# Kernel optimization log

Measured on AMD Instinct MI355X. Metric: run time of the kernel, lower is better.

The kernel has to match this reference:

```python
import jax, jax.numpy as jnp
import numpy as np

B, S, D, H = 8, 1024, 1024, 16
HD = D // H  # head dim = 64


def setup_inputs() -> dict:
    key = jax.random.key(0)
    ks = jax.random.split(key, 8)
    return {
        "hidden_states": jax.random.normal(ks[0], (B, S, D), dtype=jnp.float32),
        "attention_mask": jnp.zeros((B, 1, 1, S), dtype=jnp.float32),
        "Wq": jax.random.normal(ks[1], (D, D), dtype=jnp.float32) * (1.0 / np.sqrt(D)),
        "bq": jax.random.normal(ks[2], (D,), dtype=jnp.float32) * 0.02,
        "Wk": jax.random.normal(ks[3], (D, D), dtype=jnp.float32) * (1.0 / np.sqrt(D)),
        "bk": jax.random.normal(ks[4], (D,), dtype=jnp.float32) * 0.02,
        "Wv": jax.random.normal(ks[5], (D, D), dtype=jnp.float32) * (1.0 / np.sqrt(D)),
        "bv": jax.random.normal(ks[6], (D,), dtype=jnp.float32) * 0.02,
    }


def _split_heads(x):
    # [B,S,D] -> [B,H,S,HD]
    return x.reshape(B, S, H, HD).transpose(0, 2, 1, 3)


def reference(hidden_states, attention_mask, Wq, bq, Wk, bk, Wv, bv):
    q = _split_heads(hidden_states @ Wq + bq)
    k = _split_heads(hidden_states @ Wk + bk)
    v = _split_heads(hidden_states @ Wv + bv)
    # [B,H,S,S]
    scores = jnp.einsum("bhqd,bhkd->bhqk", q, k) / jnp.sqrt(jnp.float32(HD))
    scores = scores + attention_mask
    probs = jax.nn.softmax(scores, axis=-1)  # dropout p=0.0 (eval)
    ctx = jnp.einsum("bhqk,bhkd->bhqd", probs, v)
    # [B,H,S,HD] -> [B,S,D]
    return ctx.transpose(0, 2, 1, 3).reshape(B, S, D)
```

## Files before the change

kernel.cpp:

```cpp
#include <hip/hip_runtime.h>
#include <stdint.h>

#define BB 8
#define SS 1024
#define DD 1024
#define HH 16
#define HDIM 64

typedef __bf16 bf16x8 __attribute__((ext_vector_type(8)));
typedef float f32x4 __attribute__((ext_vector_type(4)));

__device__ __forceinline__ unsigned short f2bf(float f) {
    union { float f; unsigned u; } v; v.f = f;
    unsigned r = v.u + 0x7fff + ((v.u >> 16) & 1);
    return (unsigned short)(r >> 16);
}

__device__ __forceinline__ float exp2fast(float x) {
#if __has_builtin(__builtin_amdgcn_exp2f)
    return __builtin_amdgcn_exp2f(x);
#else
    return __expf(x * 0.69314718f);
#endif
}

__device__ __forceinline__ void async16(void* lds, const void* g) {
    __builtin_amdgcn_global_load_lds(
        (const __attribute__((address_space(1))) unsigned int*)g,
        (__attribute__((address_space(3))) unsigned int*)lds, 16, 0, 0);
}

__global__ __launch_bounds__(256) void prep(
    const float* __restrict__ x, unsigned short* __restrict__ xf,
    const float* __restrict__ w0, const float* __restrict__ w1,
    const float* __restrict__ w2,
    unsigned short* __restrict__ f0, unsigned short* __restrict__ f1,
    unsigned short* __restrict__ f2)
{
    __shared__ unsigned short tile[64 * 76];
    int bid = blockIdx.x;
    int tid = threadIdx.x;
    if (bid < 2048) {
        int mt = bid >> 4, kt = bid & 15;
        const float* src = x + (size_t)(mt * 64) * DD + kt * 64;
        #pragma unroll
        for (int i = 0; i < 4; ++i) {
            int f = tid + i * 256;
            int r = f >> 4, c4 = f & 15;
            float4 v = *reinterpret_cast<const float4*>(src + r * DD + c4 * 4);
            ushort4 o;
            o.x = f2bf(v.x); o.y = f2bf(v.y); o.z = f2bf(v.z); o.w = f2bf(v.w);
            *reinterpret_cast<ushort4*>(&tile[r * 76 + c4 * 4]) = o;
        }
        __syncthreads();
        #pragma unroll
        for (int i = 0; i < 2; ++i) {
            int s = tid + i * 256;
            int frag = s >> 6, l = s & 63;
            int m_l = (frag & 3) * 16 + (l & 15);
            int k_l = (frag >> 2) * 32 + ((l >> 4) & 3) * 8;
            uint4 v = *reinterpret_cast<const uint4*>(&tile[m_l * 76 + k_l]);
            int fm = mt * 4 + (frag & 3);
            int fk = kt * 2 + (frag >> 2);
            *reinterpret_cast<uint4*>(xf + (size_t)((fm * 32 + fk) * 64 + l) * 8) = v;
        }
        return;
    }
    int idx = bid - 2048;
    int z = idx >> 8, rem = idx & 255;
    const float* w = (z == 0) ? w0 : (z == 1) ? w1 : w2;
    unsigned short* wf = (z == 0) ? f0 : (z == 1) ? f1 : f2;
    int kt = rem & 15, nt = rem >> 4;
    const float* src = w + (size_t)(kt * 64) * DD + nt * 64;
    #pragma unroll
    for (int i = 0; i < 4; ++i) {
        int f = tid + i * 256;
        int r = f >> 4, c4 = f & 15;
        float4 v = *reinterpret_cast<const float4*>(src + r * DD + c4 * 4);
        ushort4 o;
        o.x = f2bf(v.x); o.y = f2bf(v.y); o.z = f2bf(v.z); o.w = f2bf(v.w);
        *reinterpret_cast<ushort4*>(&tile[r * 76 + c4 * 4]) = o;
    }
    __syncthreads();
    #pragma unroll
    for (int i = 0; i < 2; ++i) {
        int s = tid + i * 256;
        int frag = s >> 6, l = s & 63;
        int n_l = (frag & 3) * 16 + (l & 15);
        int k_l = (frag >> 2) * 32 + ((l >> 4) & 3) * 8;
        unsigned short tmp[8];
        #pragma unroll
        for (int j = 0; j < 8; ++j) tmp[j] = tile[(k_l + j) * 76 + n_l];
        int fn = nt * 4 + (frag & 3);
        int fk = kt * 2 + (frag >> 2);
        *reinterpret_cast<uint4*>(wf + (size_t)((fn * 32 + fk) * 64 + l) * 8) =
            *reinterpret_cast<const uint4*>(tmp);
    }
}

__global__ __launch_bounds__(256, 3) void gemm_qkv(
    const unsigned short* __restrict__ xf,
    const unsigned short* __restrict__ wf0, const unsigned short* __restrict__ wf1,
    const unsigned short* __restrict__ wf2,
    const float* __restrict__ b0, const float* __restrict__ b1, const float* __restrict__ b2,
    unsigned short* __restrict__ qo, unsigned short* __restrict__ ko,
    unsigned short* __restrict__ vto)
{
    int bid = blockIdx.x;
    int xcd = bid & 7, g = bid >> 3;
    int strip = xcd * 3 + (g % 3);
    int mt = g / 3;
    int nt = strip & 7, z = strip >> 3;

    const unsigned short* wf; const float* bias; unsigned short* out;
    if (z == 0)      { wf = wf0; bias = b0; out = qo; }
    else if (z == 1) { wf = wf1; bias = b1; out = ko; }
    else             { wf = wf2; bias = b2; out = vto; }

    __shared__ unsigned short stg[4][64 * 76];

    int tid = threadIdx.x;
    int wave = tid >> 6, lane = tid & 63, lq = lane >> 4, lm = lane & 15;
    int wr = wave >> 1, wc = wave & 1;

    const unsigned short* aB = xf + (size_t)((mt * 8 + wr * 4) * 32) * 512 + lane * 8;
    const unsigned short* bB = wf + (size_t)((nt * 8 + wc * 4) * 32) * 512 + lane * 8;

    f32x4 acc[4][4] = {};
    bf16x8 a0[4], a1[4], bb0[4], bb1[4];

#define LDFRAGS(AB, BB, T)                                                     \
    {                                                                          \
        _Pragma("unroll") for (int i_ = 0; i_ < 4; ++i_)                       \
            AB[i_] = *reinterpret_cast<const bf16x8*>(aB + (i_ * 32 + (T)) * 512); \
        _Pragma("unroll") for (int j_ = 0; j_ < 4; ++j_)                       \
            BB[j_] = *reinterpret_cast<const bf16x8*>(bB + (j_ * 32 + (T)) * 512); \
    }
#define MFMAS(AB, BB)                                                          \
    {                                                                          \
        _Pragma("unroll") for (int i_ = 0; i_ < 4; ++i_)                       \
            _Pragma("unroll") for (int j_ = 0; j_ < 4; ++j_)                   \
                acc[i_][j_] = __builtin_amdgcn_mfma_f32_16x16x32_bf16(         \
                    AB[i_], BB[j_], acc[i_][j_], 0, 0, 0);                     \
    }

    LDFRAGS(a0, bb0, 0);
    for (int tt = 0; tt < 16; ++tt) {
        int t = tt * 2;
        LDFRAGS(a1, bb1, t + 1);
        MFMAS(a0, bb0);
        LDFRAGS(a0, bb0, t + 2);
        MFMAS(a1, bb1);
    }
#undef LDFRAGS
#undef MFMAS

    int m0 = mt * 128;
    int col0 = nt * 128 + wc * 64;
    if (z == 2) {
        #pragma unroll
        for (int j = 0; j < 4; ++j) {
            int col = col0 + j * 16 + lm;
            float bsv = bias[col];
            int h = col >> 6, hd = col & 63;
            #pragma unroll
            for (int i = 0; i < 4; ++i) {
                int m = m0 + wr * 64 + i * 16 + lq * 4;
                int b_ = m >> 10, sr = m & 1023;
                union { float f; unsigned u; } p0, p1, p2, p3;
                p0.f = acc[i][j][0] + bsv; p1.f = acc[i][j][1] + bsv;
                p2.f = acc[i][j][2] + bsv; p3.f = acc[i][j][3] + bsv;
                uint2 pk;
                pk.x = __builtin_amdgcn_perm(p1.u + 0x8000u, p0.u + 0x8000u, 0x07060302u);
                pk.y = __builtin_amdgcn_perm(p3.u + 0x8000u, p2.u + 0x8000u, 0x07060302u);
                *reinterpret_cast<uint2*>(out + (((b_ * HH + h) * HDIM + hd) << 10) + sr) = pk;
            }
        }
    } else {
        unsigned short* S = stg[wave];
        #pragma unroll
        for (int j = 0; j < 4; ++j) {
            float bsv = bias[col0 + j * 16 + lm];
            #pragma unroll
            for (int i = 0; i < 4; ++i) {
                #pragma unroll
                for (int r = 0; r < 4; ++r) {
                    union { float f; unsigned u; } cv; cv.f = acc[i][j][r] + bsv;
                    S[(i * 16 + lq * 4 + r) * 76 + j * 16 + lm] =
                        (unsigned short)((cv.u + 0x8000u) >> 16);
                }
            }
        }
        int h = col0 >> 6;
        int mrow = m0 + wr * 64;
        int b_ = mrow >> 10, sr0 = mrow & 1023;
        unsigned short* ob = out + ((size_t)((b_ * HH + h) << 10) + sr0) * HDIM;
        #pragma unroll
        for (int u = 0; u < 8; ++u) {
            int s = lane + u * 64;
            int row = s >> 3, c8 = s & 7;
            uint4 v = *reinterpret_cast<const uint4*>(&S[row * 76 + c8 * 8]);
            *reinterpret_cast<uint4*>(ob + row * HDIM + c8 * 8) = v;
        }
    }
}

__global__ __launch_bounds__(256) void attention(
    const unsigned short* __restrict__ q,
    const unsigned short* __restrict__ k,
    const unsigned short* __restrict__ vt,
    const float* __restrict__ mask,
    float* __restrict__ out)
{
    __shared__ unsigned short Ks[2][64 * 64];
    __shared__ unsigned short Vs[2][64 * 64];
    __shared__ unsigned short Ps[4][16 * 72];
    __shared__ float msk[SS];

    int blk = blockIdx.x;
    int xcd = blk & 7, j = blk >> 3;
    int bh = (xcd << 4) + (j >> 4);
    int qt = j & 15;
    int b = bh >> 4, h = bh & 15;

    int tid = threadIdx.x;
    int wave = tid >> 6, lane = tid & 63, lq = lane >> 4, lm = lane & 15;

    const unsigned short* qp = q + (size_t)bh * SS * HDIM;
    const unsigned short* kp = k + (size_t)bh * SS * HDIM;
    const unsigned short* vp = vt + (size_t)bh * HDIM * SS;

    for (int i = tid; i < SS; i += 256) msk[i] = mask[b * SS + i] * 1.44269504f;

    int qrow = qt * 64 + wave * 16 + lm;
    bf16x8 qa0 = *reinterpret_cast<const bf16x8*>(qp + qrow * HDIM + lq * 8);
    bf16x8 qa1 = *reinterpret_cast<const bf16x8*>(qp + qrow * HDIM + 32 + lq * 8);

    float lsum = 0.f;
    f32x4 o[4] = {};

    int row0 = tid >> 3, sg = tid & 7;
    int cg = (sg - row0) & 7;
    const unsigned short* gk = kp + row0 * 64 + cg * 8;
    const unsigned short* gv = vp + row0 * SS + cg * 8;

    int sl0 = ((lq + lm) & 7) * 8;
    int sl1 = ((lq + lm + 4) & 7) * 8;

    async16(&Ks[0][tid * 8], gk);  async16(&Ks[0][(tid + 256) * 8], gk + 32 * 64);
    async16(&Vs[0][tid * 8], gv);  async16(&Vs[0][(tid + 256) * 8], gv + 32 * SS);
    gk += 64 * 64; gv += 64;

    unsigned short* Pw = Ps[wave];

    for (int t = 0; t < 16; ++t) {
        int p = t & 1;
        __syncthreads();
        if (t < 15) {
            async16(&Ks[p ^ 1][tid * 8], gk);  async16(&Ks[p ^ 1][(tid + 256) * 8], gk + 32 * 64);
            async16(&Vs[p ^ 1][tid * 8], gv);  async16(&Vs[p ^ 1][(tid + 256) * 8], gv + 32 * SS);
            gk += 64 * 64; gv += 64;
        }
        int kb0 = t * 64;

        f32x4 c[4];
        #pragma unroll
        for (int nb = 0; nb < 4; ++nb) {
            bf16x8 kf0 = *reinterpret_cast<const bf16x8*>(&Ks[p][(nb * 16 + lm) * 64 + sl0]);
            bf16x8 kf1 = *reinterpret_cast<const bf16x8*>(&Ks[p][(nb * 16 + lm) * 64 + sl1]);
            f32x4 z = {};
            z = __builtin_amdgcn_mfma_f32_16x16x32_bf16(kf0, qa0, z, 0, 0, 0);
            z = __builtin_amdgcn_mfma_f32_16x16x32_bf16(kf1, qa1, z, 0, 0, 0);
            c[nb] = z;
        }

        #pragma unroll
        for (int nb = 0; nb < 4; ++nb) {
            float4 mk = *reinterpret_cast<const float4*>(&msk[kb0 + nb * 16 + lq * 4]);
            unsigned u[4];
            #pragma unroll
            for (int r = 0; r < 4; ++r) {
                float e = exp2fast(fmaf(c[nb][r], 0.18033688f,
                                        reinterpret_cast<const float*>(&mk)[r]));
                union { float f; unsigned v; } cv; cv.f = e;
                u[r] = cv.v;
                union { unsigned v; float f; } tr; tr.v = cv.v & 0xffff0000u;
                lsum += tr.f;
            }
            uint2 pk;
            pk.x = __builtin_amdgcn_perm(u[1], u[0], 0x07060302u);
            pk.y = __builtin_amdgcn_perm(u[3], u[2], 0x07060302u);
            *reinterpret_cast<uint2*>(&Pw[lm * 72 + nb * 16 + lq * 4]) = pk;
        }

        #pragma unroll
        for (int ks = 0; ks < 2; ++ks) {
            bf16x8 pa = *reinterpret_cast<const bf16x8*>(&Pw[lm * 72 + ks * 32 + lq * 8]);
            int slv = (ks == 0) ? sl0 : sl1;
            #pragma unroll
            for (int nb2 = 0; nb2 < 4; ++nb2) {
                bf16x8 vf = *reinterpret_cast<const bf16x8*>(&Vs[p][(nb2 * 16 + lm) * 64 + slv]);
                o[nb2] = __builtin_amdgcn_mfma_f32_16x16x32_bf16(pa, vf, o[nb2], 0, 0, 0);
            }
        }
    }

    lsum += __shfl_xor(lsum, 16, 64);
    lsum += __shfl_xor(lsum, 32, 64);
    float linv[4];
    #pragma unroll
    for (int r = 0; r < 4; ++r)
        linv[r] = 1.0f / __shfl(lsum, lq * 4 + r, 64);

    #pragma unroll
    for (int nb2 = 0; nb2 < 4; ++nb2) {
        #pragma unroll
        for (int r = 0; r < 4; ++r) {
            int sr = qt * 64 + wave * 16 + lq * 4 + r;
            out[((size_t)(b * SS + sr)) * DD + h * HDIM + nb2 * 16 + lm] = o[nb2][r] * linv[r];
        }
    }
}

extern "C" void kernel_launch(void* const* d_in, const int* in_sizes, int n_in,
                              void* d_out, int out_size, void* d_ws, size_t ws_size,
                              hipStream_t stream) {
    const float* hs   = (const float*)d_in[0];
    const float* mask = (const float*)d_in[1];
    const float* Wq   = (const float*)d_in[2];
    const float* bq   = (const float*)d_in[3];
    const float* Wk   = (const float*)d_in[4];
    const float* bk   = (const float*)d_in[5];
    const float* Wv   = (const float*)d_in[6];
    const float* bv   = (const float*)d_in[7];
    float* out = (float*)d_out;

    char* ws = (char*)d_ws;
    unsigned short* XF  = (unsigned short*)(ws);
    unsigned short* WF0 = (unsigned short*)(ws + 16777216);
    unsigned short* WF1 = (unsigned short*)(ws + 18874368);
    unsigned short* WF2 = (unsigned short*)(ws + 20971520);
    unsigned short* qw  = (unsigned short*)(ws + 23068672);
    unsigned short* kw  = (unsigned short*)(ws + 39845888);
    unsigned short* vtw = (unsigned short*)(ws + 56623104);

    prep<<<2816, 256, 0, stream>>>(hs, XF, Wq, Wk, Wv, WF0, WF1, WF2);
    gemm_qkv<<<1536, 256, 0, stream>>>(XF, WF0, WF1, WF2,
                                       bq, bk, bv, qw, kw, vtw);
    attention<<<2048, 256, 0, stream>>>(qw, kw, vtw, mask, out);
}
```

Baseline: 232.6 us.

## Process two query tiles per attention block to halve K/V staging traffic

Each attention block now handles 128 query rows (two 16-row groups per wave) instead of 64, so every K/V tile staged in shared memory feeds twice as many MFMAs, and the grid is halved. The mask is read from global memory each iteration instead of being cached in shared memory. The P scratch buffer is narrowed to a 64-wide row with an XOR-style swizzle in place of 72-wide padding. A launch-bounds occupancy hint is added. The extra accumulators raise register pressure, and the smaller grid gives fewer blocks to fill the GPU.

```diff
diff --git a/kernel.cpp b/kernel.cpp
--- a/kernel.cpp
+++ b/kernel.cpp
@@ -205,7 +205,7 @@
     }
 }
 
-__global__ __launch_bounds__(256) void attention(
+__global__ __launch_bounds__(256, 4) void attention(
     const unsigned short* __restrict__ q,
     const unsigned short* __restrict__ k,
     const unsigned short* __restrict__ vt,
@@ -214,13 +214,12 @@
 {
     __shared__ unsigned short Ks[2][64 * 64];
     __shared__ unsigned short Vs[2][64 * 64];
-    __shared__ unsigned short Ps[4][16 * 72];
-    __shared__ float msk[SS];
+    __shared__ unsigned short Ps[4][16 * 64];
 
     int blk = blockIdx.x;
     int xcd = blk & 7, j = blk >> 3;
-    int bh = (xcd << 4) + (j >> 4);
-    int qt = j & 15;
+    int bh = (xcd << 4) + (j >> 3);
+    int qt = j & 7;
     int b = bh >> 4, h = bh & 15;
 
     int tid = threadIdx.x;
@@ -229,15 +228,16 @@
     const unsigned short* qp = q + (size_t)bh * SS * HDIM;
     const unsigned short* kp = k + (size_t)bh * SS * HDIM;
     const unsigned short* vp = vt + (size_t)bh * HDIM * SS;
-
-    for (int i = tid; i < SS; i += 256) msk[i] = mask[b * SS + i] * 1.44269504f;
-
-    int qrow = qt * 64 + wave * 16 + lm;
-    bf16x8 qa0 = *reinterpret_cast<const bf16x8*>(qp + qrow * HDIM + lq * 8);
-    bf16x8 qa1 = *reinterpret_cast<const bf16x8*>(qp + qrow * HDIM + 32 + lq * 8);
-
-    float lsum = 0.f;
-    f32x4 o[4] = {};
+    const float* maskb = mask + b * SS;
+
+    int qbase = qt * 128 + wave * 16 + lm;
+    bf16x8 qa00 = *reinterpret_cast<const bf16x8*>(qp + qbase * HDIM + lq * 8);
+    bf16x8 qa01 = *reinterpret_cast<const bf16x8*>(qp + qbase * HDIM + 32 + lq * 8);
+    bf16x8 qa10 = *reinterpret_cast<const bf16x8*>(qp + (qbase + 64) * HDIM + lq * 8);
+    bf16x8 qa11 = *reinterpret_cast<const bf16x8*>(qp + (qbase + 64) * HDIM + 32 + lq * 8);
+
+    float lsum0 = 0.f, lsum1 = 0.f;
+    f32x4 o0[4] = {}, o1[4] = {};
 
     int row0 = tid >> 3, sg = tid & 7;
     int cg = (sg - row0) & 7;
@@ -246,78 +246,123 @@
 
     int sl0 = ((lq + lm) & 7) * 8;
     int sl1 = ((lq + lm + 4) & 7) * 8;
+    unsigned short* Pw = Ps[wave];
+    int pwbase = lm * 64 + (lq & 1) * 4;
+    int prd0 = lm * 64 + sl0;
+    int prd1 = lm * 64 + sl1;
 
     async16(&Ks[0][tid * 8], gk);  async16(&Ks[0][(tid + 256) * 8], gk + 32 * 64);
     async16(&Vs[0][tid * 8], gv);  async16(&Vs[0][(tid + 256) * 8], gv + 32 * SS);
     gk += 64 * 64; gv += 64;
 
-    unsigned short* Pw = Ps[wave];
-
     for (int t = 0; t < 16; ++t) {
         int p = t & 1;
         __syncthreads();
+        int kb0 = t * 64;
+
+        float4 mk[4];
+        #pragma unroll
+        for (int nb = 0; nb < 4; ++nb) {
+            mk[nb] = *reinterpret_cast<const float4*>(maskb + kb0 + nb * 16 + lq * 4);
+            #pragma unroll
+            for (int r = 0; r < 4; ++r)
+                reinterpret_cast<float*>(&mk[nb])[r] *= 1.44269504f;
+        }
         if (t < 15) {
             async16(&Ks[p ^ 1][tid * 8], gk);  async16(&Ks[p ^ 1][(tid + 256) * 8], gk + 32 * 64);
             async16(&Vs[p ^ 1][tid * 8], gv);  async16(&Vs[p ^ 1][(tid + 256) * 8], gv + 32 * SS);
             gk += 64 * 64; gv += 64;
         }
-        int kb0 = t * 64;
-
-        f32x4 c[4];
+
+        f32x4 c0[4], c1[4];
         #pragma unroll
         for (int nb = 0; nb < 4; ++nb) {
             bf16x8 kf0 = *reinterpret_cast<const bf16x8*>(&Ks[p][(nb * 16 + lm) * 64 + sl0]);
             bf16x8 kf1 = *reinterpret_cast<const bf16x8*>(&Ks[p][(nb * 16 + lm) * 64 + sl1]);
             f32x4 z = {};
-            z = __builtin_amdgcn_mfma_f32_16x16x32_bf16(kf0, qa0, z, 0, 0, 0);
-            z = __builtin_amdgcn_mfma_f32_16x16x32_bf16(kf1, qa1, z, 0, 0, 0);
-            c[nb] = z;
+            z = __builtin_amdgcn_mfma_f32_16x16x32_bf16(kf0, qa00, z, 0, 0, 0);
+            z = __builtin_amdgcn_mfma_f32_16x16x32_bf16(kf1, qa01, z, 0, 0, 0);
+            c0[nb] = z;
+            f32x4 w = {};
+            w = __builtin_amdgcn_mfma_f32_16x16x32_bf16(kf0, qa10, w, 0, 0, 0);
+            w = __builtin_amdgcn_mfma_f32_16x16x32_bf16(kf1, qa11, w, 0, 0, 0);
+            c1[nb] = w;
         }
 
         #pragma unroll
         for (int nb = 0; nb < 4; ++nb) {
-            float4 mk = *reinterpret_cast<const float4*>(&msk[kb0 + nb * 16 + lq * 4]);
             unsigned u[4];
             #pragma unroll
             for (int r = 0; r < 4; ++r) {
-                float e = exp2fast(fmaf(c[nb][r], 0.18033688f,
-                                        reinterpret_cast<const float*>(&mk)[r]));
+                float e = exp2fast(fmaf(c0[nb][r], 0.18033688f,
+                                        reinterpret_cast<const float*>(&mk[nb])[r]));
                 union { float f; unsigned v; } cv; cv.f = e;
                 u[r] = cv.v;
                 union { unsigned v; float f; } tr; tr.v = cv.v & 0xffff0000u;
-                lsum += tr.f;
+                lsum0 += tr.f;
             }
             uint2 pk;
             pk.x = __builtin_amdgcn_perm(u[1], u[0], 0x07060302u);
             pk.y = __builtin_amdgcn_perm(u[3], u[2], 0x07060302u);
-            *reinterpret_cast<uint2*>(&Pw[lm * 72 + nb * 16 + lq * 4]) = pk;
-        }
-
-        #pragma unroll
-        for (int ks = 0; ks < 2; ++ks) {
-            bf16x8 pa = *reinterpret_cast<const bf16x8*>(&Pw[lm * 72 + ks * 32 + lq * 8]);
-            int slv = (ks == 0) ? sl0 : sl1;
-            #pragma unroll
-            for (int nb2 = 0; nb2 < 4; ++nb2) {
-                bf16x8 vf = *reinterpret_cast<const bf16x8*>(&Vs[p][(nb2 * 16 + lm) * 64 + slv]);
-                o[nb2] = __builtin_amdgcn_mfma_f32_16x16x32_bf16(pa, vf, o[nb2], 0, 0, 0);
+            *reinterpret_cast<uint2*>(
+                &Pw[pwbase + (((nb * 2 + (lq >> 1)) + lm) & 7) * 8]) = pk;
+        }
+        bf16x8 pa00 = *reinterpret_cast<const bf16x8*>(&Pw[prd0]);
+        bf16x8 pa01 = *reinterpret_cast<const bf16x8*>(&Pw[prd1]);
+
+        #pragma unroll
+        for (int nb = 0; nb < 4; ++nb) {
+            unsigned u[4];
+            #pragma unroll
+            for (int r = 0; r < 4; ++r) {
+                float e = exp2fast(fmaf(c1[nb][r], 0.18033688f,
+                                        reinterpret_cast<const float*>(&mk[nb])[r]));
+                union { float f; unsigned v; } cv; cv.f = e;
+                u[r] = cv.v;
+                union { unsigned v; float f; } tr; tr.v = cv.v & 0xffff0000u;
+                lsum1 += tr.f;
             }
-        }
-    }
-
-    lsum += __shfl_xor(lsum, 16, 64);
-    lsum += __shfl_xor(lsum, 32, 64);
-    float linv[4];
+            uint2 pk;
+            pk.x = __builtin_amdgcn_perm(u[1], u[0], 0x07060302u);
+            pk.y = __builtin_amdgcn_perm(u[3], u[2], 0x07060302u);
+            *reinterpret_cast<uint2*>(
+                &Pw[pwbase + (((nb * 2 + (lq >> 1)) + lm) & 7) * 8]) = pk;
+        }
+        bf16x8 pa10 = *reinterpret_cast<const bf16x8*>(&Pw[prd0]);
+        bf16x8 pa11 = *reinterpret_cast<const bf16x8*>(&Pw[prd1]);
+
+        #pragma unroll
+        for (int nb2 = 0; nb2 < 4; ++nb2) {
+            bf16x8 vf0 = *reinterpret_cast<const bf16x8*>(&Vs[p][(nb2 * 16 + lm) * 64 + sl0]);
+            o0[nb2] = __builtin_amdgcn_mfma_f32_16x16x32_bf16(pa00, vf0, o0[nb2], 0, 0, 0);
+            o1[nb2] = __builtin_amdgcn_mfma_f32_16x16x32_bf16(pa10, vf0, o1[nb2], 0, 0, 0);
+            bf16x8 vf1 = *reinterpret_cast<const bf16x8*>(&Vs[p][(nb2 * 16 + lm) * 64 + sl1]);
+            o0[nb2] = __builtin_amdgcn_mfma_f32_16x16x32_bf16(pa01, vf1, o0[nb2], 0, 0, 0);
+            o1[nb2] = __builtin_amdgcn_mfma_f32_16x16x32_bf16(pa11, vf1, o1[nb2], 0, 0, 0);
+        }
+    }
+
+    lsum0 += __shfl_xor(lsum0, 16, 64);
+    lsum0 += __shfl_xor(lsum0, 32, 64);
+    lsum1 += __shfl_xor(lsum1, 16, 64);
+    lsum1 += __shfl_xor(lsum1, 32, 64);
+    float linv0[4], linv1[4];
     #pragma unroll
-    for (int r = 0; r < 4; ++r)
-        linv[r] = 1.0f / __shfl(lsum, lq * 4 + r, 64);
-
+    for (int r = 0; r < 4; ++r) {
+        linv0[r] = 1.0f / __shfl(lsum0, lq * 4 + r, 64);
+        linv1[r] = 1.0f / __shfl(lsum1, lq * 4 + r, 64);
+    }
+
+    int srb = qt * 128 + wave * 16;
     #pragma unroll
     for (int nb2 = 0; nb2 < 4; ++nb2) {
         #pragma unroll
         for (int r = 0; r < 4; ++r) {
-            int sr = qt * 64 + wave * 16 + lq * 4 + r;
-            out[((size_t)(b * SS + sr)) * DD + h * HDIM + nb2 * 16 + lm] = o[nb2][r] * linv[r];
+            int sr = srb + lq * 4 + r;
+            out[((size_t)(b * SS + sr)) * DD + h * HDIM + nb2 * 16 + lm] =
+                o0[nb2][r] * linv0[r];
+            out[((size_t)(b * SS + sr + 64)) * DD + h * HDIM + nb2 * 16 + lm] =
+                o1[nb2][r] * linv1[r];
         }
     }
 }
@@ -347,5 +392,5 @@
     prep<<<2816, 256, 0, stream>>>(hs, XF, Wq, Wk, Wv, WF0, WF1, WF2);
     gemm_qkv<<<1536, 256, 0, stream>>>(XF, WF0, WF1, WF2,
                                        bq, bk, bv, qw, kw, vtw);
-    attention<<<2048, 256, 0, stream>>>(qw, kw, vtw, mask, out);
-}
+    attention<<<1024, 256, 0, stream>>>(qw, kw, vtw, mask, out);
+}
```

Measured after the change: 218.2 us. -6.2%, faster.
